# Kernel optimization log

Measured on AMD Instinct MI355X. Metric: run time of the kernel, lower is better.

The kernel has to match this reference:

```python
import jax, jax.numpy as jnp
import numpy as np

HEADS = 4

def _layernorm(x, g, b, eps=1e-5):
    mu = x.mean(-1, keepdims=True)
    var = ((x - mu) ** 2).mean(-1, keepdims=True)
    return (x - mu) / jnp.sqrt(var + eps) * g + b

def _feature_map(data, proj, is_query, eps=1e-4):
    # FAVOR+ softmax kernel features. data: [B,H,S,dh], proj: [m,dh]
    dh = data.shape[-1]
    m = proj.shape[0]
    dn = dh ** -0.25
    ratio = m ** -0.5
    dash = jnp.einsum('bhsd,md->bhsm', data * dn, proj)
    diag = 0.5 * jnp.sum((data * dn) ** 2, axis=-1, keepdims=True)
    mx = jnp.max(dash, axis=-1, keepdims=True) if is_query else jnp.max(dash)
    return ratio * (jnp.exp(dash - diag - mx) + eps)

def _causal_linear_attention(q, k, v):
    # q,k: [B,H,S,m] kernel features; v: [B,H,S,dh]
    k_cum = jnp.cumsum(k, axis=2)                                  # [B,H,S,m]
    d_inv = 1.0 / jnp.einsum('bhsm,bhsm->bhs', q, k_cum)           # [B,H,S]
    ctx = jnp.cumsum(jnp.einsum('bhsm,bhsd->bhsmd', k, v), axis=2) # [B,H,S,m,dh]
    return jnp.einsum('bhsmd,bhsm,bhs->bhsd', ctx, q, d_inv)

def reference(x, pre_w, pre_b, ln1_g, ln1_b, wq, wk, wv, wo, bo, proj,
              ln2_g, ln2_b, ff_w1, ff_b1, ff_w2, ff_b2, tgt_w, tgt_b, rd_w, rd_b):
    # preproc: 1x1x1 conv3d + softplus
    xbn = jax.nn.softplus(jnp.einsum('bcthw,oc->bothw', x, pre_w)
                          + pre_b[None, :, None, None, None])
    B, D, T, H, W = xbn.shape
    tokens = xbn.reshape(B, -1, D)  # raw torch-style reshape, S = T*H*W
    S = tokens.shape[1]

    # Performer block (depth=1): prenorm attention + prenorm FF, residuals
    h = _layernorm(tokens, ln1_g, ln1_b)
    split = lambda t: t.reshape(B, S, HEADS, -1).transpose(0, 2, 1, 3)
    q, k, v = split(h @ wq), split(h @ wk), split(h @ wv)
    qp = _feature_map(q, proj, True)
    kp = _feature_map(k, proj, False)
    attn = _causal_linear_attention(qp, kp, v)
    attn = attn.transpose(0, 2, 1, 3).reshape(B, S, D)
    tokens = tokens + attn @ wo + bo
    h2 = _layernorm(tokens, ln2_g, ln2_b)
    tokens = tokens + jax.nn.gelu(h2 @ ff_w1 + ff_b1, approximate=False) @ ff_w2 + ff_b2

    # readout
    out = tokens.reshape(B, D, T, H, W).mean(axis=2)               # [B,D,H,W]
    out = jnp.concatenate([out, x[:, 2, 0][:, None]], axis=1)      # [B,D+1,H,W]
    out = jax.lax.conv_general_dilated(out, tgt_w, (1, 1), [(2, 2), (2, 2)],
                                       dimension_numbers=('NCHW', 'OIHW', 'NCHW'))
    out = out + tgt_b[None, :, None, None]
    out = out.mean(axis=(2, 3))                                    # global avg pool -> [B,1]
    return out @ rd_w.T + rd_b


def setup_inputs() -> dict:
    key = jax.random.key(0)
    ks = jax.random.split(key, 12)
    B, T, H, W = 2, 8, 48, 48
    D, DH, M, FF = 64, 16, 32, 256
    s = lambda k, shape, sc=1.0: jax.random.normal(k, shape, jnp.float32) * sc
    inv = 1.0 / np.sqrt(D)
    return {
        'x': s(ks[0], (B, 3, T, H, W)),
        'pre_w': s(ks[1], (D, 3), 1.0 / np.sqrt(3)),
        'pre_b': jnp.zeros((D,), jnp.float32),
        'ln1_g': jnp.ones((D,), jnp.float32), 'ln1_b': jnp.zeros((D,), jnp.float32),
        'wq': s(ks[2], (D, D), inv), 'wk': s(ks[3], (D, D), inv), 'wv': s(ks[4], (D, D), inv),
        'wo': s(ks[5], (D, D), inv), 'bo': jnp.zeros((D,), jnp.float32),
        'proj': s(ks[6], (M, DH)),
        'ln2_g': jnp.ones((D,), jnp.float32), 'ln2_b': jnp.zeros((D,), jnp.float32),
        'ff_w1': s(ks[7], (D, FF), inv), 'ff_b1': jnp.zeros((FF,), jnp.float32),
        'ff_w2': s(ks[8], (FF, D), 1.0 / np.sqrt(FF)), 'ff_b2': jnp.zeros((D,), jnp.float32),
        'tgt_w': s(ks[9], (1, D + 1, 5, 5), 1.0 / np.sqrt((D + 1) * 25)),
        'tgt_b': jnp.zeros((1,), jnp.float32),
        'rd_w': s(ks[10], (1, 1)), 'rd_b': jnp.zeros((1,), jnp.float32),
    }
```

## Files before the change

kernel.cpp:

```cpp
#include <hip/hip_runtime.h>
#include <hip/hip_bf16.h>
#include <math.h>

typedef __hip_bfloat16 bf16;
typedef __attribute__((ext_vector_type(8))) short short8;
typedef __attribute__((ext_vector_type(16))) float floatx16;

constexpr int B_   = 2;
constexpr int T_   = 8;
constexpr int HW   = 48 * 48;
constexpr int S_   = T_ * HW;
constexpr int D_   = 64;
constexpr int NH   = 4;
constexpr int DH   = 16;
constexpr int M_   = 32;
constexpr int BS   = B_ * S_;
constexpr int BSD  = BS * D_;
constexpr int BH   = B_ * NH;
constexpr int BHS  = BH * S_;
constexpr int BHSM = BHS * M_;
constexpr int CHUNK = 32;
constexpr int NC   = S_ / CHUNK;
constexpr int STATE = M_ * DH + M_;
constexpr float DN = 0.5f;
constexpr float RATIO = 0.17677669529663687f;

__device__ __forceinline__ unsigned short f2bf(float f) {
  bf16 h = __float2bfloat16(f);
  return *reinterpret_cast<unsigned short*>(&h);
}

__global__ void k_preln(const float* __restrict__ x, const float* __restrict__ pw,
                        const float* __restrict__ pb, const float* __restrict__ g,
                        const float* __restrict__ bb,
                        float* __restrict__ tok, float* __restrict__ h) {
  int token = blockIdx.x * 4 + (threadIdx.x >> 6);
  int lane = threadIdx.x & 63;
  int f = token * 64 + lane;
  int b = f / (D_ * S_);
  int r = f % (D_ * S_);
  int d = r / S_;
  int pos = r % S_;
  const float* xb = x + b * 3 * S_ + pos;
  float a = xb[0] * pw[d * 3 + 0] + xb[S_] * pw[d * 3 + 1] + xb[2 * S_] * pw[d * 3 + 2]
          + pb[d];
  float t = fmaxf(a, 0.f) + log1pf(expf(-fabsf(a)));
  tok[f] = t;
  float s1 = t, s2 = t * t;
  for (int off = 32; off; off >>= 1) {
    s1 += __shfl_xor(s1, off);
    s2 += __shfl_xor(s2, off);
  }
  float mu = s1 * (1.f / 64.f);
  float var = s2 * (1.f / 64.f) - mu * mu;
  float rs = rsqrtf(var + 1e-5f);
  h[f] = (t - mu) * rs * g[lane] + bb[lane];
}

__global__ void __launch_bounds__(192) k_qkv(const float* __restrict__ h,
                      const float* __restrict__ wq, const float* __restrict__ wk,
                      const float* __restrict__ wv,
                      float* __restrict__ q, float* __restrict__ k, float* __restrict__ v) {
  int tid = threadIdx.x;
  int w = tid >> 6;
  int L = tid & 63;
  int half = L >> 5;
  int n = L & 31;
  int tbase = blockIdx.x * 32;
  const float* wm = (w == 0) ? wq : (w == 1) ? wk : wv;
  float* outm = (w == 0) ? q : (w == 1) ? k : v;

  short8 a[4];
  {
    const float* hrow = h + (size_t)(tbase + n) * 64 + half * 8;
#pragma unroll
    for (int c = 0; c < 4; ++c) {
      float4 f0 = *(const float4*)&hrow[c * 16];
      float4 f1 = *(const float4*)&hrow[c * 16 + 4];
      a[c][0] = (short)f2bf(f0.x); a[c][1] = (short)f2bf(f0.y);
      a[c][2] = (short)f2bf(f0.z); a[c][3] = (short)f2bf(f0.w);
      a[c][4] = (short)f2bf(f1.x); a[c][5] = (short)f2bf(f1.y);
      a[c][6] = (short)f2bf(f1.z); a[c][7] = (short)f2bf(f1.w);
    }
  }
#pragma unroll
  for (int ct = 0; ct < 2; ++ct) {
    int col = ct * 32 + n;
    short8 bfrag[4];
#pragma unroll
    for (int c = 0; c < 4; ++c) {
#pragma unroll
      for (int j = 0; j < 8; ++j)
        bfrag[c][j] = (short)f2bf(wm[(c * 16 + half * 8 + j) * 64 + col]);
    }
    floatx16 acc;
#pragma unroll
    for (int i = 0; i < 16; ++i) acc[i] = 0.f;
    acc = __builtin_amdgcn_mfma_f32_32x32x16_bf16(a[0], bfrag[0], acc, 0, 0, 0);
    acc = __builtin_amdgcn_mfma_f32_32x32x16_bf16(a[1], bfrag[1], acc, 0, 0, 0);
    acc = __builtin_amdgcn_mfma_f32_32x32x16_bf16(a[2], bfrag[2], acc, 0, 0, 0);
    acc = __builtin_amdgcn_mfma_f32_32x32x16_bf16(a[3], bfrag[3], acc, 0, 0, 0);
    int head = col >> 4, di = col & 15;
#pragma unroll
    for (int r = 0; r < 16; ++r) {
      int row = (r & 3) + 8 * (r >> 2) + 4 * half;
      int token = tbase + row;
      int b = token / S_, s = token % S_;
      outm[((size_t)(b * NH + head) * S_ + s) * DH + di] = acc[r];
    }
  }
}

__global__ void __launch_bounds__(64) k_feat(const float* __restrict__ q,
                      const float* __restrict__ k, const float* __restrict__ proj,
                      bf16* __restrict__ qpb, float* __restrict__ kp,
                      float* __restrict__ diagk, float* __restrict__ part) {
  __shared__ __align__(16) float sPT[16 * 32];
  int tid = threadIdx.x;
  for (int e = tid; e < 512; e += 64) {
    int d = e >> 5, m = e & 31;
    sPT[d * 32 + m] = proj[m * 16 + d];
  }
  __syncthreads();
  int row = blockIdx.x * 64 + tid;
  float qv[16], kv[16];
  float dq = 0.f, dk = 0.f;
  {
    const float4* q4 = (const float4*)(q + (size_t)row * 16);
    const float4* k4 = (const float4*)(k + (size_t)row * 16);
#pragma unroll
    for (int i = 0; i < 4; ++i) {
      float4 t4 = q4[i];
      qv[4*i] = t4.x * DN; qv[4*i+1] = t4.y * DN; qv[4*i+2] = t4.z * DN; qv[4*i+3] = t4.w * DN;
      float4 u4 = k4[i];
      kv[4*i] = u4.x * DN; kv[4*i+1] = u4.y * DN; kv[4*i+2] = u4.z * DN; kv[4*i+3] = u4.w * DN;
    }
#pragma unroll
    for (int d = 0; d < 16; ++d) { dq += qv[d] * qv[d]; dk += kv[d] * kv[d]; }
    dq *= 0.5f; dk *= 0.5f;
  }
  float accq[32], acck[32];
#pragma unroll
  for (int m = 0; m < 32; ++m) { accq[m] = 0.f; acck[m] = 0.f; }
#pragma unroll
  for (int d = 0; d < 16; ++d) {
    float qd = qv[d], kd = kv[d];
    const float4* pr = (const float4*)&sPT[d * 32];
#pragma unroll
    for (int m4 = 0; m4 < 8; ++m4) {
      float4 p = pr[m4];
      accq[4*m4+0] += qd * p.x; accq[4*m4+1] += qd * p.y;
      accq[4*m4+2] += qd * p.z; accq[4*m4+3] += qd * p.w;
      acck[4*m4+0] += kd * p.x; acck[4*m4+1] += kd * p.y;
      acck[4*m4+2] += kd * p.z; acck[4*m4+3] += kd * p.w;
    }
  }
  float mx = accq[0];
#pragma unroll
  for (int m = 1; m < 32; ++m) mx = fmaxf(mx, accq[m]);
#pragma unroll
  for (int m8 = 0; m8 < 4; ++m8) {
    float o[8];
#pragma unroll
    for (int j = 0; j < 8; ++j)
      o[j] = RATIO * (expf(accq[m8 * 8 + j] - dq - mx) + 1e-4f);
    uint4 pk;
    pk.x = (unsigned)f2bf(o[0]) | ((unsigned)f2bf(o[1]) << 16);
    pk.y = (unsigned)f2bf(o[2]) | ((unsigned)f2bf(o[3]) << 16);
    pk.z = (unsigned)f2bf(o[4]) | ((unsigned)f2bf(o[5]) << 16);
    pk.w = (unsigned)f2bf(o[6]) | ((unsigned)f2bf(o[7]) << 16);
    *(uint4*)&qpb[(size_t)row * 32 + m8 * 8] = pk;
  }
  float bmax = acck[0];
#pragma unroll
  for (int m = 1; m < 32; ++m) bmax = fmaxf(bmax, acck[m]);
#pragma unroll
  for (int m4 = 0; m4 < 8; ++m4)
    *(float4*)&kp[(size_t)row * 32 + m4 * 4] = *(float4*)&acck[4 * m4];
  diagk[row] = dk;
  for (int off = 32; off; off >>= 1) bmax = fmaxf(bmax, __shfl_xor(bmax, off));
  if (tid == 0) part[blockIdx.x] = bmax;
}

__global__ void k_maxred(const float* __restrict__ part, float* __restrict__ gmax) {
  float m = -3.4e38f;
  for (int i = threadIdx.x; i < BHS / 64; i += 256) m = fmaxf(m, part[i]);
  __shared__ float red[256];
  red[threadIdx.x] = m;
  __syncthreads();
  for (int s = 128; s; s >>= 1) {
    if (threadIdx.x < s) red[threadIdx.x] = fmaxf(red[threadIdx.x], red[threadIdx.x + s]);
    __syncthreads();
  }
  if (!threadIdx.x) gmax[0] = red[0];
}

__global__ void __launch_bounds__(256) k_csfin(const float* __restrict__ diagk,
                      const float* __restrict__ gmax, const float* __restrict__ v,
                      const float* __restrict__ kp, bf16* __restrict__ kpb,
                      float* __restrict__ ckv) {
  __shared__ __align__(16) float sKp[CHUNK * 32];
  __shared__ __align__(16) float sVc[CHUNK * 16];
  int blk = blockIdx.x;
  int bh = blk / NC, c = blk % NC;
  int tid = threadIdx.x;
  int base = bh * S_ + c * CHUNK;
  float gm = gmax[0];
  {
    int row = tid >> 3, m4 = tid & 7;
    float4 dash = *(const float4*)&kp[(size_t)(base + row) * 32 + m4 * 4];
    float dg = diagk[base + row] + gm;
    float4 fin;
    fin.x = RATIO * (expf(dash.x - dg) + 1e-4f);
    fin.y = RATIO * (expf(dash.y - dg) + 1e-4f);
    fin.z = RATIO * (expf(dash.z - dg) + 1e-4f);
    fin.w = RATIO * (expf(dash.w - dg) + 1e-4f);
    *(float4*)&sKp[row * 32 + m4 * 4] = fin;
    uint2 u;
    u.x = (unsigned)f2bf(fin.x) | ((unsigned)f2bf(fin.y) << 16);
    u.y = (unsigned)f2bf(fin.z) | ((unsigned)f2bf(fin.w) << 16);
    *(uint2*)&kpb[(size_t)(base + row) * 32 + m4 * 4] = u;
  }
  if (tid < 128) {
    int row = tid >> 2, c4 = tid & 3;
    *(float4*)&sVc[row * 16 + c4 * 4] = *(const float4*)&v[(size_t)(base + row) * 16 + c4 * 4];
  }
  __syncthreads();
  int m0 = tid >> 4, d0 = tid & 15;
  int m1 = m0 + 16;
  float a0 = 0.f, a1 = 0.f, az0 = 0.f, az1 = 0.f;
  for (int t = 0; t < CHUNK; ++t) {
    float k0 = sKp[t * 32 + m0];
    float k1 = sKp[t * 32 + m1];
    float vv = sVc[t * 16 + d0];
    a0 += k0 * vv;
    a1 += k1 * vv;
    if (d0 == 0) { az0 += k0; az1 += k1; }
  }
  float* outp = ckv + (size_t)blk * STATE;
  outp[m0 * 16 + d0] = a0;
  outp[m1 * 16 + d0] = a1;
  if (d0 == 0) { outp[512 + m0] = az0; outp[512 + m1] = az1; }
}

__global__ void k_prefix(float* __restrict__ ckv) {
  int idx = blockIdx.x * 256 + threadIdx.x;
  int bh = idx / STATE, c = idx % STATE;
  float run = 0.f;
  for (int j0 = 0; j0 < NC; j0 += 16) {
    float tb[16];
#pragma unroll
    for (int jj = 0; jj < 16; ++jj) tb[jj] = ckv[((size_t)bh * NC + j0 + jj) * STATE + c];
#pragma unroll
    for (int jj = 0; jj < 16; ++jj) {
      ckv[((size_t)bh * NC + j0 + jj) * STATE + c] = run;
      run += tb[jj];
    }
  }
}

__global__ void __launch_bounds__(256) k_attn(const bf16* __restrict__ qpb,
                                              const bf16* __restrict__ kpb,
                                              const float* __restrict__ v,
                                              const float* __restrict__ ckv,
                                              float* __restrict__ attn) {
  __shared__ __align__(16) float sP[4][32 * 33 + 4];
  int tid = threadIdx.x;
  int w = tid >> 6;
  int L = tid & 63;
  int half = L >> 5;
  int n = L & 31;
  int chunk = blockIdx.x * 4 + w;
  int bh = chunk / NC, c = chunk % NC;
  int base = bh * S_ + c * CHUNK;

  short8 a1 = *(const short8*)(qpb + (size_t)(base + n) * 32 + half * 8);
  short8 a2 = *(const short8*)(qpb + (size_t)(base + n) * 32 + 16 + half * 8);
  short8 b1 = *(const short8*)(kpb + (size_t)(base + n) * 32 + half * 8);
  short8 b2 = *(const short8*)(kpb + (size_t)(base + n) * 32 + 16 + half * 8);

  floatx16 P;
#pragma unroll
  for (int i = 0; i < 16; ++i) P[i] = 0.f;
  P = __builtin_amdgcn_mfma_f32_32x32x16_bf16(a1, b1, P, 0, 0, 0);
  P = __builtin_amdgcn_mfma_f32_32x32x16_bf16(a2, b2, P, 0, 0, 0);

  float* sp = &sP[w][0];
#pragma unroll
  for (int r = 0; r < 16; ++r) {
    int i = (r & 3) + 8 * (r >> 2) + 4 * half;
    sp[i * 33 + n] = (n <= i) ? P[r] : 0.f;
  }
  __syncthreads();
  short8 pa1, pa2;
#pragma unroll
  for (int j = 0; j < 8; ++j) {
    pa1[j] = (short)f2bf(sp[n * 33 + half * 8 + j]);
    pa2[j] = (short)f2bf(sp[n * 33 + 16 + half * 8 + j]);
  }

  const float* cs = ckv + (size_t)chunk * STATE;
  short8 vb1, vb2, sb1, sb2;
#pragma unroll
  for (int j = 0; j < 8; ++j) {
    int t1 = half * 8 + j, t2 = 16 + half * 8 + j;
    float x1 = (n < 16) ? v[(size_t)(base + t1) * 16 + n] : (n == 16 ? 1.f : 0.f);
    float x2 = (n < 16) ? v[(size_t)(base + t2) * 16 + n] : (n == 16 ? 1.f : 0.f);
    vb1[j] = (short)f2bf(x1);
    vb2[j] = (short)f2bf(x2);
    float y1 = (n < 16) ? cs[t1 * 16 + n] : (n == 16 ? cs[512 + t1] : 0.f);
    float y2 = (n < 16) ? cs[t2 * 16 + n] : (n == 16 ? cs[512 + t2] : 0.f);
    sb1[j] = (short)f2bf(y1);
    sb2[j] = (short)f2bf(y2);
  }

  floatx16 O;
#pragma unroll
  for (int i = 0; i < 16; ++i) O[i] = 0.f;
  O = __builtin_amdgcn_mfma_f32_32x32x16_bf16(pa1, vb1, O, 0, 0, 0);
  O = __builtin_amdgcn_mfma_f32_32x32x16_bf16(pa2, vb2, O, 0, 0, 0);
  O = __builtin_amdgcn_mfma_f32_32x32x16_bf16(a1, sb1, O, 0, 0, 0);
  O = __builtin_amdgcn_mfma_f32_32x32x16_bf16(a2, sb2, O, 0, 0, 0);

  int srcl = 16 + 32 * half;
  float res[16];
#pragma unroll
  for (int r = 0; r < 16; ++r) {
    float den = __shfl(O[r], srcl, 64);
    res[r] = O[r] / den;
  }
  if (n < 16) {
    int b = bh >> 2, head = bh & 3;
#pragma unroll
    for (int r = 0; r < 16; ++r) {
      int i = (r & 3) + 8 * (r >> 2) + 4 * half;
      attn[((size_t)(b * S_ + c * CHUNK + i)) * 64 + head * 16 + n] = res[r];
    }
  }
}

__global__ void __launch_bounds__(128) k_wo_ln(const float* __restrict__ attn,
                        const float* __restrict__ wo, const float* __restrict__ bo,
                        const float* __restrict__ tok, const float* __restrict__ g,
                        const float* __restrict__ bb,
                        float* __restrict__ tok2, float* __restrict__ h2) {
  __shared__ __align__(16) float sC[32 * 68];
  int tid = threadIdx.x;
  int w = tid >> 6;
  int L = tid & 63;
  int half = L >> 5;
  int n = L & 31;
  int tbase = blockIdx.x * 32;

  short8 a[4];
  {
    const float* arow = attn + (size_t)(tbase + n) * 64 + half * 8;
#pragma unroll
    for (int c = 0; c < 4; ++c) {
      float4 f0 = *(const float4*)&arow[c * 16];
      float4 f1 = *(const float4*)&arow[c * 16 + 4];
      a[c][0] = (short)f2bf(f0.x); a[c][1] = (short)f2bf(f0.y);
      a[c][2] = (short)f2bf(f0.z); a[c][3] = (short)f2bf(f0.w);
      a[c][4] = (short)f2bf(f1.x); a[c][5] = (short)f2bf(f1.y);
      a[c][6] = (short)f2bf(f1.z); a[c][7] = (short)f2bf(f1.w);
    }
  }
  int col = w * 32 + n;
  short8 bfrag[4];
#pragma unroll
  for (int c = 0; c < 4; ++c) {
#pragma unroll
    for (int j = 0; j < 8; ++j)
      bfrag[c][j] = (short)f2bf(wo[(c * 16 + half * 8 + j) * 64 + col]);
  }
  floatx16 acc;
#pragma unroll
  for (int i = 0; i < 16; ++i) acc[i] = 0.f;
  acc = __builtin_amdgcn_mfma_f32_32x32x16_bf16(a[0], bfrag[0], acc, 0, 0, 0);
  acc = __builtin_amdgcn_mfma_f32_32x32x16_bf16(a[1], bfrag[1], acc, 0, 0, 0);
  acc = __builtin_amdgcn_mfma_f32_32x32x16_bf16(a[2], bfrag[2], acc, 0, 0, 0);
  acc = __builtin_amdgcn_mfma_f32_32x32x16_bf16(a[3], bfrag[3], acc, 0, 0, 0);
  float bias = bo[col];
#pragma unroll
  for (int r = 0; r < 16; ++r) {
    int row = (r & 3) + 8 * (r >> 2) + 4 * half;
    sC[row * 68 + col] = acc[r] + tok[(size_t)(tbase + row) * 64 + col] + bias;
  }
  __syncthreads();
  int tg = tid >> 5, cg = tid & 31;
  int c0 = cg * 2, c1 = c0 + 1;
  float g0 = g[c0], g1 = g[c1], be0 = bb[c0], be1 = bb[c1];
#pragma unroll
  for (int i = 0; i < 8; ++i) {
    int lrow = tg * 8 + i;
    int token = tbase + lrow;
    float t0 = sC[lrow * 68 + c0];
    float t1 = sC[lrow * 68 + c1];
    float s1 = t0 + t1, s2 = t0 * t0 + t1 * t1;
    for (int off = 16; off; off >>= 1) {
      s1 += __shfl_xor(s1, off, 32);
      s2 += __shfl_xor(s2, off, 32);
    }
    float mu = s1 * (1.f / 64.f);
    float var = s2 * (1.f / 64.f) - mu * mu;
    float rs = rsqrtf(var + 1e-5f);
    tok2[token * 64 + c0] = t0;
    tok2[token * 64 + c1] = t1;
    h2[token * 64 + c0] = (t0 - mu) * rs * g0 + be0;
    h2[token * 64 + c1] = (t1 - mu) * rs * g1 + be1;
  }
}

__global__ void __launch_bounds__(256) k_ffg(const float* __restrict__ h2,
                                             const float* __restrict__ w1,
                                             const float* __restrict__ b1,
                                             float* __restrict__ Gavg) {
  int tid = threadIdx.x;
  int w = tid >> 6;
  int L = tid & 63;
  int half = L >> 5;
  int n = L & 31;
  int blk = blockIdx.x;
  int b = blk / 576;
  int rem = blk % 576;
  int ch = rem / 9;
  int jp0 = (rem % 9) * 4;
  int token_n = b * 18432 + ch * 288 + (n & 7) * 36 + jp0 + (n >> 3);

  short8 a[4];
  {
    const float* hrow = h2 + (size_t)token_n * 64 + half * 8;
#pragma unroll
    for (int c = 0; c < 4; ++c) {
      float4 f0 = *(const float4*)&hrow[c * 16];
      float4 f1 = *(const float4*)&hrow[c * 16 + 4];
      a[c][0] = (short)f2bf(f0.x); a[c][1] = (short)f2bf(f0.y);
      a[c][2] = (short)f2bf(f0.z); a[c][3] = (short)f2bf(f0.w);
      a[c][4] = (short)f2bf(f1.x); a[c][5] = (short)f2bf(f1.y);
      a[c][6] = (short)f2bf(f1.z); a[c][7] = (short)f2bf(f1.w);
    }
  }
  size_t gbase = ((size_t)(b * 64 + ch) * 36 + jp0);
#pragma unroll
  for (int ct = 0; ct < 2; ++ct) {
    int col = w * 64 + ct * 32 + n;
    short8 bfrag[4];
#pragma unroll
    for (int c = 0; c < 4; ++c) {
#pragma unroll
      for (int j = 0; j < 8; ++j)
        bfrag[c][j] = (short)f2bf(w1[(c * 16 + half * 8 + j) * 256 + col]);
    }
    floatx16 acc;
#pragma unroll
    for (int i = 0; i < 16; ++i) acc[i] = 0.f;
    acc = __builtin_amdgcn_mfma_f32_32x32x16_bf16(a[0], bfrag[0], acc, 0, 0, 0);
    acc = __builtin_amdgcn_mfma_f32_32x32x16_bf16(a[1], bfrag[1], acc, 0, 0, 0);
    acc = __builtin_amdgcn_mfma_f32_32x32x16_bf16(a[2], bfrag[2], acc, 0, 0, 0);
    acc = __builtin_amdgcn_mfma_f32_32x32x16_bf16(a[3], bfrag[3], acc, 0, 0, 0);
    float bias = b1[col];
#pragma unroll
    for (int j = 0; j < 4; ++j) {
      float s = 0.f;
#pragma unroll
      for (int rr = 0; rr < 4; ++rr) {
        float xg = acc[j * 4 + rr] + bias;
        s += 0.5f * xg * (1.f + erff(xg * 0.70710678118654752f));
      }
      s += __shfl_xor(s, 32);
      if (half == 0)
        Gavg[(gbase + j) * 256 + col] = s * 0.125f;
    }
  }
}

__global__ void __launch_bounds__(256) k_pool2(const float* __restrict__ Gavg,
                        const float* __restrict__ tok2, const float* __restrict__ w2,
                        const float* __restrict__ b2, float* __restrict__ pool) {
  __shared__ __align__(16) float sG[18 * 256];
  __shared__ __align__(16) float sRed[4 * 18 * 64];
  int blk = blockIdx.x;
  int b = blk / 128;
  int rem = blk % 128;
  int ch = rem >> 1, jph = rem & 1;
  int tid = threadIdx.x;
  size_t grow0 = ((size_t)(b * 64 + ch) * 36 + jph * 18) * 256;
  for (int e = tid; e < 1152; e += 256) {
    int row = e >> 6, c4 = e & 63;
    *(float4*)&sG[row * 256 + c4 * 4] = *(const float4*)&Gavg[grow0 + row * 256 + c4 * 4];
  }
  __syncthreads();
  int kg = tid >> 6, dd = tid & 63;
  float acc[18];
#pragma unroll
  for (int i = 0; i < 18; ++i) acc[i] = 0.f;
  for (int k4 = 0; k4 < 16; ++k4) {
    int k = kg * 64 + k4 * 4;
    float w0 = w2[(k + 0) * 64 + dd];
    float w1 = w2[(k + 1) * 64 + dd];
    float w2v = w2[(k + 2) * 64 + dd];
    float w3 = w2[(k + 3) * 64 + dd];
#pragma unroll
    for (int i = 0; i < 18; ++i) {
      float4 gf = *(const float4*)&sG[i * 256 + k];
      acc[i] += gf.x * w0 + gf.y * w1 + gf.z * w2v + gf.w * w3;
    }
  }
#pragma unroll
  for (int i = 0; i < 18; ++i) sRed[(kg * 18 + i) * 64 + dd] = acc[i];
  __syncthreads();
  for (int o = tid; o < 1152; o += 256) {
    int jp18 = o >> 6, d2 = o & 63;
    float gsum = sRed[(0 * 18 + jp18) * 64 + d2] + sRed[(1 * 18 + jp18) * 64 + d2]
               + sRed[(2 * 18 + jp18) * 64 + d2] + sRed[(3 * 18 + jp18) * 64 + d2];
    int p = (jph * 18 + jp18) * 64 + d2;
    size_t tbase = (size_t)b * 1179648 + (size_t)ch * 18432 + p;
    float ts = 0.f;
#pragma unroll
    for (int t = 0; t < 8; ++t) ts += tok2[tbase + t * 2304];
    pool[((size_t)(b * 64 + ch)) * HW + p] = ts * 0.125f + gsum + b2[d2];
  }
}

__global__ void __launch_bounds__(256) k_convsum(const float* __restrict__ pool,
                                                 const float* __restrict__ x,
                                                 const float* __restrict__ w,
                                                 float* __restrict__ partial) {
  int blk = blockIdx.x;
  int b = blk / 65, ch = blk % 65;
  int tid = threadIdx.x;
  __shared__ float cls[25];
  __shared__ float red[256];
  if (tid < 25) {
    int ry = tid / 5, rx = tid % 5;
    int kh0 = (ry <= 2) ? 0 : (ry == 3 ? 1 : 2);
    int kh1 = (ry >= 2) ? 4 : (ry == 1 ? 3 : 2);
    int kw0 = (rx <= 2) ? 0 : (rx == 3 ? 1 : 2);
    int kw1 = (rx >= 2) ? 4 : (rx == 1 ? 3 : 2);
    float s = 0.f;
    for (int kh = kh0; kh <= kh1; ++kh)
      for (int kw = kw0; kw <= kw1; ++kw)
        s += w[ch * 25 + kh * 5 + kw];
    cls[tid] = s;
  }
  __syncthreads();
  const float* pc = (ch < 64) ? (pool + ((size_t)(b * 64 + ch)) * HW)
                              : (x + (size_t)b * 3 * S_ + 2 * S_);
  float acc = 0.f;
#pragma unroll
  for (int e = tid; e < HW; e += 256) {
    int iy = e / 48, ix = e % 48;
    int ry = (iy == 0) ? 0 : (iy == 1) ? 1 : (iy <= 45) ? 2 : (iy == 46) ? 3 : 4;
    int rx = (ix == 0) ? 0 : (ix == 1) ? 1 : (ix <= 45) ? 2 : (ix == 46) ? 3 : 4;
    acc += pc[e] * cls[ry * 5 + rx];
  }
  red[tid] = acc;
  __syncthreads();
  for (int s = 128; s; s >>= 1) {
    if (tid < s) red[tid] += red[tid + s];
    __syncthreads();
  }
  if (!tid) partial[blk] = red[0];
}

__global__ void k_final(const float* __restrict__ partial, const float* __restrict__ tgt_b,
                        const float* __restrict__ rd_w, const float* __restrict__ rd_b,
                        float* __restrict__ out) {
  int b = blockIdx.x;
  int lane = threadIdx.x;
  float s = (lane < 65) ? partial[b * 65 + lane] : 0.f;
  for (int off = 32; off; off >>= 1) s += __shfl_down(s, off, 64);
  __shared__ float r2;
  if (lane == 64) r2 = s;
  __syncthreads();
  if (!lane) {
    float tot = s + r2;
    float mean = tot / 2304.f + tgt_b[0];
    out[b] = mean * rd_w[0] + rd_b[0];
  }
}

extern "C" void kernel_launch(void* const* d_in, const int* in_sizes, int n_in,
                              void* d_out, int out_size, void* d_ws, size_t ws_size,
                              hipStream_t stream) {
  const float* x     = (const float*)d_in[0];
  const float* pre_w = (const float*)d_in[1];
  const float* pre_b = (const float*)d_in[2];
  const float* ln1_g = (const float*)d_in[3];
  const float* ln1_b = (const float*)d_in[4];
  const float* wq    = (const float*)d_in[5];
  const float* wk    = (const float*)d_in[6];
  const float* wv    = (const float*)d_in[7];
  const float* wo    = (const float*)d_in[8];
  const float* bo    = (const float*)d_in[9];
  const float* proj  = (const float*)d_in[10];
  const float* ln2_g = (const float*)d_in[11];
  const float* ln2_b = (const float*)d_in[12];
  const float* ff_w1 = (const float*)d_in[13];
  const float* ff_b1 = (const float*)d_in[14];
  const float* ff_w2 = (const float*)d_in[15];
  const float* ff_b2 = (const float*)d_in[16];
  const float* tgt_w = (const float*)d_in[17];
  const float* tgt_b = (const float*)d_in[18];
  const float* rd_w  = (const float*)d_in[19];
  const float* rd_b  = (const float*)d_in[20];
  float* out = (float*)d_out;

  float* ws = (float*)d_ws;
  float* tok   = ws;
  float* v     = ws + (size_t)BSD;
  float* q     = ws + 2 * (size_t)BSD;
  float* Gavg  = ws + 2 * (size_t)BSD;
  float* pool  = Gavg + 1179648;
  float* k     = ws + 3 * (size_t)BSD;
  float* h     = ws + 4 * (size_t)BSD;
  float* kp    = ws + 4 * (size_t)BSD;
  bf16*  qpb   = (bf16*)(ws + 6 * (size_t)BSD);
  bf16*  kpb   = (bf16*)(ws + 7 * (size_t)BSD);
  float* ckv   = ws + 8 * (size_t)BSD;
  float* tok2  = ws + 8 * (size_t)BSD;
  float* attnb = k;
  float* h2    = ws + 4 * (size_t)BSD;
  float* smalls = ws + 9 * (size_t)BSD + 147456;
  float* diagk = smalls;
  float* part  = diagk + BHS;
  float* gmax  = part + BHSM / 256;
  float* partial = gmax + 64;

  k_preln<<<dim3(BS / 4), dim3(256), 0, stream>>>(x, pre_w, pre_b, ln1_g, ln1_b, tok, h);
  k_qkv<<<dim3(BS / 32), dim3(192), 0, stream>>>(h, wq, wk, wv, q, k, v);
  k_feat<<<dim3(BHS / 64), dim3(64), 0, stream>>>(q, k, proj, qpb, kp, diagk, part);
  k_maxred<<<dim3(1), dim3(256), 0, stream>>>(part, gmax);
  k_csfin<<<dim3(BH * NC), dim3(256), 0, stream>>>(diagk, gmax, v, kp, kpb, ckv);
  k_prefix<<<dim3(BH * STATE / 256), dim3(256), 0, stream>>>(ckv);
  k_attn<<<dim3(BH * NC / 4), dim3(256), 0, stream>>>(qpb, kpb, v, ckv, attnb);
  k_wo_ln<<<dim3(BS / 32), dim3(128), 0, stream>>>(attnb, wo, bo, tok, ln2_g, ln2_b, tok2, h2);
  k_ffg<<<dim3(B_ * 64 * 9), dim3(256), 0, stream>>>(h2, ff_w1, ff_b1, Gavg);
  k_pool2<<<dim3(B_ * 64 * 2), dim3(256), 0, stream>>>(Gavg, tok2, ff_w2, ff_b2, pool);
  k_convsum<<<dim3(B_ * 65), dim3(256), 0, stream>>>(pool, x, tgt_w, partial);
  k_final<<<dim3(B_), dim3(128), 0, stream>>>(partial, tgt_b, rd_w, rd_b, out);
}
```

Measured before the change: 240.4 us.

## Fuse global max via atomics, recompute key features, merge pool and conv readout

```diff
diff --git a/kernel.cpp b/kernel.cpp
--- a/kernel.cpp
+++ b/kernel.cpp
@@ -29,11 +29,24 @@
   bf16 h = __float2bfloat16(f);
   return *reinterpret_cast<unsigned short*>(&h);
 }
+__device__ __forceinline__ unsigned encmax(float f) {
+  unsigned u = __float_as_uint(f);
+  return (u & 0x80000000u) ? ~u : (u | 0x80000000u);
+}
+__device__ __forceinline__ float decmax(unsigned e) {
+  unsigned u = (e & 0x80000000u) ? (e ^ 0x80000000u) : ~e;
+  return __uint_as_float(u);
+}
 
 __global__ void k_preln(const float* __restrict__ x, const float* __restrict__ pw,
                         const float* __restrict__ pb, const float* __restrict__ g,
                         const float* __restrict__ bb,
-                        float* __restrict__ tok, float* __restrict__ h) {
+                        float* __restrict__ tok, float* __restrict__ h,
+                        float* __restrict__ partial, unsigned* __restrict__ gmaxu) {
+  if (blockIdx.x == 0) {
+    if (threadIdx.x < 130) partial[threadIdx.x] = 0.f;
+    if (threadIdx.x == 200) gmaxu[0] = 0u;
+  }
   int token = blockIdx.x * 4 + (threadIdx.x >> 6);
   int lane = threadIdx.x & 63;
   int f = token * 64 + lane;
@@ -113,8 +126,7 @@
 
 __global__ void __launch_bounds__(64) k_feat(const float* __restrict__ q,
                       const float* __restrict__ k, const float* __restrict__ proj,
-                      bf16* __restrict__ qpb, float* __restrict__ kp,
-                      float* __restrict__ diagk, float* __restrict__ part) {
+                      bf16* __restrict__ qpb, unsigned* __restrict__ gmaxu) {
   __shared__ __align__(16) float sPT[16 * 32];
   int tid = threadIdx.x;
   for (int e = tid; e < 512; e += 64) {
@@ -124,7 +136,7 @@
   __syncthreads();
   int row = blockIdx.x * 64 + tid;
   float qv[16], kv[16];
-  float dq = 0.f, dk = 0.f;
+  float dq = 0.f;
   {
     const float4* q4 = (const float4*)(q + (size_t)row * 16);
     const float4* k4 = (const float4*)(k + (size_t)row * 16);
@@ -136,8 +148,8 @@
       kv[4*i] = u4.x * DN; kv[4*i+1] = u4.y * DN; kv[4*i+2] = u4.z * DN; kv[4*i+3] = u4.w * DN;
     }
 #pragma unroll
-    for (int d = 0; d < 16; ++d) { dq += qv[d] * qv[d]; dk += kv[d] * kv[d]; }
-    dq *= 0.5f; dk *= 0.5f;
+    for (int d = 0; d < 16; ++d) dq += qv[d] * qv[d];
+    dq *= 0.5f;
   }
   float accq[32], acck[32];
 #pragma unroll
@@ -174,73 +186,78 @@
   float bmax = acck[0];
 #pragma unroll
   for (int m = 1; m < 32; ++m) bmax = fmaxf(bmax, acck[m]);
-#pragma unroll
-  for (int m4 = 0; m4 < 8; ++m4)
-    *(float4*)&kp[(size_t)row * 32 + m4 * 4] = *(float4*)&acck[4 * m4];
-  diagk[row] = dk;
   for (int off = 32; off; off >>= 1) bmax = fmaxf(bmax, __shfl_xor(bmax, off));
-  if (tid == 0) part[blockIdx.x] = bmax;
-}
-
-__global__ void k_maxred(const float* __restrict__ part, float* __restrict__ gmax) {
-  float m = -3.4e38f;
-  for (int i = threadIdx.x; i < BHS / 64; i += 256) m = fmaxf(m, part[i]);
-  __shared__ float red[256];
-  red[threadIdx.x] = m;
-  __syncthreads();
-  for (int s = 128; s; s >>= 1) {
-    if (threadIdx.x < s) red[threadIdx.x] = fmaxf(red[threadIdx.x], red[threadIdx.x + s]);
-    __syncthreads();
-  }
-  if (!threadIdx.x) gmax[0] = red[0];
-}
-
-__global__ void __launch_bounds__(256) k_csfin(const float* __restrict__ diagk,
-                      const float* __restrict__ gmax, const float* __restrict__ v,
-                      const float* __restrict__ kp, bf16* __restrict__ kpb,
-                      float* __restrict__ ckv) {
-  __shared__ __align__(16) float sKp[CHUNK * 32];
-  __shared__ __align__(16) float sVc[CHUNK * 16];
+  if (tid == 0) atomicMax(gmaxu, encmax(bmax));
+}
+
+__global__ void __launch_bounds__(256) k_csfin(const float* __restrict__ k,
+                      const float* __restrict__ v, const float* __restrict__ proj,
+                      const unsigned* __restrict__ gmaxu,
+                      bf16* __restrict__ kpb, float* __restrict__ ckv) {
+  __shared__ float sK[32 * 17];
+  __shared__ __align__(16) float sPT[16 * 32];
+  __shared__ float sKp[32 * 33];
+  __shared__ __align__(16) float sVc[32 * 16];
   int blk = blockIdx.x;
   int bh = blk / NC, c = blk % NC;
   int tid = threadIdx.x;
   int base = bh * S_ + c * CHUNK;
-  float gm = gmax[0];
-  {
-    int row = tid >> 3, m4 = tid & 7;
-    float4 dash = *(const float4*)&kp[(size_t)(base + row) * 32 + m4 * 4];
-    float dg = diagk[base + row] + gm;
-    float4 fin;
-    fin.x = RATIO * (expf(dash.x - dg) + 1e-4f);
-    fin.y = RATIO * (expf(dash.y - dg) + 1e-4f);
-    fin.z = RATIO * (expf(dash.z - dg) + 1e-4f);
-    fin.w = RATIO * (expf(dash.w - dg) + 1e-4f);
-    *(float4*)&sKp[row * 32 + m4 * 4] = fin;
-    uint2 u;
-    u.x = (unsigned)f2bf(fin.x) | ((unsigned)f2bf(fin.y) << 16);
-    u.y = (unsigned)f2bf(fin.z) | ((unsigned)f2bf(fin.w) << 16);
-    *(uint2*)&kpb[(size_t)(base + row) * 32 + m4 * 4] = u;
+  for (int e = tid; e < 512; e += 256) {
+    int d = e >> 5, m = e & 31;
+    sPT[d * 32 + m] = proj[m * 16 + d];
   }
   if (tid < 128) {
     int row = tid >> 2, c4 = tid & 3;
-    *(float4*)&sVc[row * 16 + c4 * 4] = *(const float4*)&v[(size_t)(base + row) * 16 + c4 * 4];
-  }
-  __syncthreads();
-  int m0 = tid >> 4, d0 = tid & 15;
+    float4 kf = *(const float4*)&k[(size_t)(base + row) * 16 + c4 * 4];
+    sK[row * 17 + c4 * 4 + 0] = kf.x;
+    sK[row * 17 + c4 * 4 + 1] = kf.y;
+    sK[row * 17 + c4 * 4 + 2] = kf.z;
+    sK[row * 17 + c4 * 4 + 3] = kf.w;
+    float4 vf = *(const float4*)&v[(size_t)(base + row) * 16 + c4 * 4];
+    *(float4*)&sVc[row * 16 + c4 * 4] = vf;
+  }
+  __syncthreads();
+  float gm = decmax(gmaxu[0]);
+  {
+    int row = tid >> 3, mq = (tid & 7) * 4;
+    float dk = 0.f, d0 = 0.f, d1 = 0.f, d2 = 0.f, d3 = 0.f;
+#pragma unroll
+    for (int d = 0; d < 16; ++d) {
+      float kd = sK[row * 17 + d] * DN;
+      dk += kd * kd;
+      const float4 p = *(const float4*)&sPT[d * 32 + mq];
+      d0 += kd * p.x; d1 += kd * p.y; d2 += kd * p.z; d3 += kd * p.w;
+    }
+    dk *= 0.5f;
+    float f0 = RATIO * (expf(d0 - dk - gm) + 1e-4f);
+    float f1 = RATIO * (expf(d1 - dk - gm) + 1e-4f);
+    float f2 = RATIO * (expf(d2 - dk - gm) + 1e-4f);
+    float f3 = RATIO * (expf(d3 - dk - gm) + 1e-4f);
+    uint2 u;
+    u.x = (unsigned)f2bf(f0) | ((unsigned)f2bf(f1) << 16);
+    u.y = (unsigned)f2bf(f2) | ((unsigned)f2bf(f3) << 16);
+    *(uint2*)&kpb[(size_t)(base + row) * 32 + mq] = u;
+    sKp[row * 33 + mq + 0] = f0;
+    sKp[row * 33 + mq + 1] = f1;
+    sKp[row * 33 + mq + 2] = f2;
+    sKp[row * 33 + mq + 3] = f3;
+  }
+  __syncthreads();
+  int m0 = tid >> 4, d0i = tid & 15;
   int m1 = m0 + 16;
   float a0 = 0.f, a1 = 0.f, az0 = 0.f, az1 = 0.f;
   for (int t = 0; t < CHUNK; ++t) {
-    float k0 = sKp[t * 32 + m0];
-    float k1 = sKp[t * 32 + m1];
-    float vv = sVc[t * 16 + d0];
+    float k0 = sKp[t * 33 + m0];
+    float k1 = sKp[t * 33 + m1];
+    float vv = sVc[t * 16 + d0i];
     a0 += k0 * vv;
     a1 += k1 * vv;
-    if (d0 == 0) { az0 += k0; az1 += k1; }
+    if (d0i == 0) { az0 += k0; az1 += k1; }
   }
   float* outp = ckv + (size_t)blk * STATE;
-  outp[m0 * 16 + d0] = a0;
-  outp[m1 * 16 + d0] = a1;
-  if (d0 == 0) { outp[512 + m0] = az0; outp[512 + m1] = az1; }
+  outp[m0 * 16 + d0i] = a0;
+  outp[m1 * 16 + d0i] = a1;
+  if (d0i == 0) { outp[512 + m0] = az0; outp[512 + m1] = az1; }
 }
 
 __global__ void k_prefix(float* __restrict__ ckv) {
@@ -474,63 +491,19 @@
   }
 }
 
-__global__ void __launch_bounds__(256) k_pool2(const float* __restrict__ Gavg,
+__global__ void __launch_bounds__(256) k_poolc(const float* __restrict__ Gavg,
                         const float* __restrict__ tok2, const float* __restrict__ w2,
-                        const float* __restrict__ b2, float* __restrict__ pool) {
+                        const float* __restrict__ b2, const float* __restrict__ tw,
+                        float* __restrict__ partial) {
   __shared__ __align__(16) float sG[18 * 256];
   __shared__ __align__(16) float sRed[4 * 18 * 64];
+  __shared__ float cls[25];
+  __shared__ float red[256];
   int blk = blockIdx.x;
   int b = blk / 128;
   int rem = blk % 128;
   int ch = rem >> 1, jph = rem & 1;
   int tid = threadIdx.x;
-  size_t grow0 = ((size_t)(b * 64 + ch) * 36 + jph * 18) * 256;
-  for (int e = tid; e < 1152; e += 256) {
-    int row = e >> 6, c4 = e & 63;
-    *(float4*)&sG[row * 256 + c4 * 4] = *(const float4*)&Gavg[grow0 + row * 256 + c4 * 4];
-  }
-  __syncthreads();
-  int kg = tid >> 6, dd = tid & 63;
-  float acc[18];
-#pragma unroll
-  for (int i = 0; i < 18; ++i) acc[i] = 0.f;
-  for (int k4 = 0; k4 < 16; ++k4) {
-    int k = kg * 64 + k4 * 4;
-    float w0 = w2[(k + 0) * 64 + dd];
-    float w1 = w2[(k + 1) * 64 + dd];
-    float w2v = w2[(k + 2) * 64 + dd];
-    float w3 = w2[(k + 3) * 64 + dd];
-#pragma unroll
-    for (int i = 0; i < 18; ++i) {
-      float4 gf = *(const float4*)&sG[i * 256 + k];
-      acc[i] += gf.x * w0 + gf.y * w1 + gf.z * w2v + gf.w * w3;
-    }
-  }
-#pragma unroll
-  for (int i = 0; i < 18; ++i) sRed[(kg * 18 + i) * 64 + dd] = acc[i];
-  __syncthreads();
-  for (int o = tid; o < 1152; o += 256) {
-    int jp18 = o >> 6, d2 = o & 63;
-    float gsum = sRed[(0 * 18 + jp18) * 64 + d2] + sRed[(1 * 18 + jp18) * 64 + d2]
-               + sRed[(2 * 18 + jp18) * 64 + d2] + sRed[(3 * 18 + jp18) * 64 + d2];
-    int p = (jph * 18 + jp18) * 64 + d2;
-    size_t tbase = (size_t)b * 1179648 + (size_t)ch * 18432 + p;
-    float ts = 0.f;
-#pragma unroll
-    for (int t = 0; t < 8; ++t) ts += tok2[tbase + t * 2304];
-    pool[((size_t)(b * 64 + ch)) * HW + p] = ts * 0.125f + gsum + b2[d2];
-  }
-}
-
-__global__ void __launch_bounds__(256) k_convsum(const float* __restrict__ pool,
-                                                 const float* __restrict__ x,
-                                                 const float* __restrict__ w,
-                                                 float* __restrict__ partial) {
-  int blk = blockIdx.x;
-  int b = blk / 65, ch = blk % 65;
-  int tid = threadIdx.x;
-  __shared__ float cls[25];
-  __shared__ float red[256];
   if (tid < 25) {
     int ry = tid / 5, rx = tid % 5;
     int kh0 = (ry <= 2) ? 0 : (ry == 3 ? 1 : 2);
@@ -540,42 +513,97 @@
     float s = 0.f;
     for (int kh = kh0; kh <= kh1; ++kh)
       for (int kw = kw0; kw <= kw1; ++kw)
-        s += w[ch * 25 + kh * 5 + kw];
+        s += tw[ch * 25 + kh * 5 + kw];
     cls[tid] = s;
   }
-  __syncthreads();
-  const float* pc = (ch < 64) ? (pool + ((size_t)(b * 64 + ch)) * HW)
-                              : (x + (size_t)b * 3 * S_ + 2 * S_);
-  float acc = 0.f;
-#pragma unroll
-  for (int e = tid; e < HW; e += 256) {
+  size_t grow0 = ((size_t)(b * 64 + ch) * 36 + jph * 18) * 256;
+  for (int e = tid; e < 1152; e += 256) {
+    int row = e >> 6, c4 = e & 63;
+    *(float4*)&sG[row * 256 + c4 * 4] = *(const float4*)&Gavg[grow0 + row * 256 + c4 * 4];
+  }
+  __syncthreads();
+  int kg = tid >> 6, dd = tid & 63;
+  float acc[18];
+#pragma unroll
+  for (int i = 0; i < 18; ++i) acc[i] = 0.f;
+  for (int k4 = 0; k4 < 16; ++k4) {
+    int k = kg * 64 + k4 * 4;
+    float w0 = w2[(k + 0) * 64 + dd];
+    float w1 = w2[(k + 1) * 64 + dd];
+    float w2v = w2[(k + 2) * 64 + dd];
+    float w3 = w2[(k + 3) * 64 + dd];
+#pragma unroll
+    for (int i = 0; i < 18; ++i) {
+      float4 gf = *(const float4*)&sG[i * 256 + k];
+      acc[i] += gf.x * w0 + gf.y * w1 + gf.z * w2v + gf.w * w3;
+    }
+  }
+#pragma unroll
+  for (int i = 0; i < 18; ++i) sRed[(kg * 18 + i) * 64 + dd] = acc[i];
+  __syncthreads();
+  float csum = 0.f;
+  for (int o = tid; o < 1152; o += 256) {
+    int jp18 = o >> 6, d2 = o & 63;
+    float gsum = sRed[(0 * 18 + jp18) * 64 + d2] + sRed[(1 * 18 + jp18) * 64 + d2]
+               + sRed[(2 * 18 + jp18) * 64 + d2] + sRed[(3 * 18 + jp18) * 64 + d2];
+    int p = (jph * 18 + jp18) * 64 + d2;
+    size_t tbase = (size_t)b * 1179648 + (size_t)ch * 18432 + p;
+    float ts = 0.f;
+#pragma unroll
+    for (int t = 0; t < 8; ++t) ts += tok2[tbase + t * 2304];
+    float val = ts * 0.125f + gsum + b2[d2];
+    int iy = p / 48, ix = p % 48;
+    int ry = (iy == 0) ? 0 : (iy == 1) ? 1 : (iy <= 45) ? 2 : (iy == 46) ? 3 : 4;
+    int rx = (ix == 0) ? 0 : (ix == 1) ? 1 : (ix <= 45) ? 2 : (ix == 46) ? 3 : 4;
+    csum += val * cls[ry * 5 + rx];
+  }
+  red[tid] = csum;
+  __syncthreads();
+  for (int s = 128; s; s >>= 1) {
+    if (tid < s) red[tid] += red[tid + s];
+    __syncthreads();
+  }
+  if (!tid) atomicAdd(&partial[b * 65 + ch], red[0]);
+}
+
+__global__ void __launch_bounds__(128) k_final(const float* __restrict__ partial,
+                        const float* __restrict__ x, const float* __restrict__ tw,
+                        const float* __restrict__ tgt_b, const float* __restrict__ rd_w,
+                        const float* __restrict__ rd_b, float* __restrict__ out) {
+  __shared__ float cls[25];
+  __shared__ float red[128];
+  int b = blockIdx.x;
+  int tid = threadIdx.x;
+  if (tid < 25) {
+    int ry = tid / 5, rx = tid % 5;
+    int kh0 = (ry <= 2) ? 0 : (ry == 3 ? 1 : 2);
+    int kh1 = (ry >= 2) ? 4 : (ry == 1 ? 3 : 2);
+    int kw0 = (rx <= 2) ? 0 : (rx == 3 ? 1 : 2);
+    int kw1 = (rx >= 2) ? 4 : (rx == 1 ? 3 : 2);
+    float s = 0.f;
+    for (int kh = kh0; kh <= kh1; ++kh)
+      for (int kw = kw0; kw <= kw1; ++kw)
+        s += tw[64 * 25 + kh * 5 + kw];
+    cls[tid] = s;
+  }
+  __syncthreads();
+  float xacc = 0.f;
+  const float* xp = x + (size_t)b * 3 * S_ + 2 * S_;
+  for (int e = tid; e < HW; e += 128) {
     int iy = e / 48, ix = e % 48;
     int ry = (iy == 0) ? 0 : (iy == 1) ? 1 : (iy <= 45) ? 2 : (iy == 46) ? 3 : 4;
     int rx = (ix == 0) ? 0 : (ix == 1) ? 1 : (ix <= 45) ? 2 : (ix == 46) ? 3 : 4;
-    acc += pc[e] * cls[ry * 5 + rx];
-  }
-  red[tid] = acc;
-  __syncthreads();
-  for (int s = 128; s; s >>= 1) {
+    xacc += xp[e] * cls[ry * 5 + rx];
+  }
+  float valv = xacc + ((tid < 64) ? partial[b * 65 + tid] : 0.f);
+  red[tid] = valv;
+  __syncthreads();
+  for (int s = 64; s; s >>= 1) {
     if (tid < s) red[tid] += red[tid + s];
     __syncthreads();
   }
-  if (!tid) partial[blk] = red[0];
-}
-
-__global__ void k_final(const float* __restrict__ partial, const float* __restrict__ tgt_b,
-                        const float* __restrict__ rd_w, const float* __restrict__ rd_b,
-                        float* __restrict__ out) {
-  int b = blockIdx.x;
-  int lane = threadIdx.x;
-  float s = (lane < 65) ? partial[b * 65 + lane] : 0.f;
-  for (int off = 32; off; off >>= 1) s += __shfl_down(s, off, 64);
-  __shared__ float r2;
-  if (lane == 64) r2 = s;
-  __syncthreads();
-  if (!lane) {
-    float tot = s + r2;
-    float mean = tot / 2304.f + tgt_b[0];
+  if (!tid) {
+    float mean = red[0] / 2304.f + tgt_b[0];
     out[b] = mean * rd_w[0] + rd_b[0];
   }
 }
@@ -611,10 +639,8 @@
   float* v     = ws + (size_t)BSD;
   float* q     = ws + 2 * (size_t)BSD;
   float* Gavg  = ws + 2 * (size_t)BSD;
-  float* pool  = Gavg + 1179648;
   float* k     = ws + 3 * (size_t)BSD;
   float* h     = ws + 4 * (size_t)BSD;
-  float* kp    = ws + 4 * (size_t)BSD;
   bf16*  qpb   = (bf16*)(ws + 6 * (size_t)BSD);
   bf16*  kpb   = (bf16*)(ws + 7 * (size_t)BSD);
   float* ckv   = ws + 8 * (size_t)BSD;
@@ -622,21 +648,18 @@
   float* attnb = k;
   float* h2    = ws + 4 * (size_t)BSD;
   float* smalls = ws + 9 * (size_t)BSD + 147456;
-  float* diagk = smalls;
-  float* part  = diagk + BHS;
-  float* gmax  = part + BHSM / 256;
-  float* partial = gmax + 64;
-
-  k_preln<<<dim3(BS / 4), dim3(256), 0, stream>>>(x, pre_w, pre_b, ln1_g, ln1_b, tok, h);
+  unsigned* gmaxu = (unsigned*)smalls;
+  float* partial  = smalls + 64;
+
+  k_preln<<<dim3(BS / 4), dim3(256), 0, stream>>>(x, pre_w, pre_b, ln1_g, ln1_b, tok, h,
+                                                  partial, gmaxu);
   k_qkv<<<dim3(BS / 32), dim3(192), 0, stream>>>(h, wq, wk, wv, q, k, v);
-  k_feat<<<dim3(BHS / 64), dim3(64), 0, stream>>>(q, k, proj, qpb, kp, diagk, part);
-  k_maxred<<<dim3(1), dim3(256), 0, stream>>>(part, gmax);
-  k_csfin<<<dim3(BH * NC), dim3(256), 0, stream>>>(diagk, gmax, v, kp, kpb, ckv);
+  k_feat<<<dim3(BHS / 64), dim3(64), 0, stream>>>(q, k, proj, qpb, gmaxu);
+  k_csfin<<<dim3(BH * NC), dim3(256), 0, stream>>>(k, v, proj, gmaxu, kpb, ckv);
   k_prefix<<<dim3(BH * STATE / 256), dim3(256), 0, stream>>>(ckv);
   k_attn<<<dim3(BH * NC / 4), dim3(256), 0, stream>>>(qpb, kpb, v, ckv, attnb);
   k_wo_ln<<<dim3(BS / 32), dim3(128), 0, stream>>>(attnb, wo, bo, tok, ln2_g, ln2_b, tok2, h2);
   k_ffg<<<dim3(B_ * 64 * 9), dim3(256), 0, stream>>>(h2, ff_w1, ff_b1, Gavg);
-  k_pool2<<<dim3(B_ * 64 * 2), dim3(256), 0, stream>>>(Gavg, tok2, ff_w2, ff_b2, pool);
-  k_convsum<<<dim3(B_ * 65), dim3(256), 0, stream>>>(pool, x, tgt_w, partial);
-  k_final<<<dim3(B_), dim3(128), 0, stream>>>(partial, tgt_b, rd_w, rd_b, out);
-}
+  k_poolc<<<dim3(B_ * 64 * 2), dim3(256), 0, stream>>>(Gavg, tok2, ff_w2, ff_b2, tgt_w, partial);
+  k_final<<<dim3(B_), dim3(128), 0, stream>>>(partial, x, tgt_w, tgt_b, rd_w, rd_b, out);
+}
```

Result: slower. 263.7 us (+9.7%).
